# Kernel tuning notes

Measured on AMD Instinct MI355X. Metric: run time of the kernel, lower is better.

The kernel has to match this reference:

```python
import jax, jax.numpy as jnp
import numpy as np

B, S, D = 128, 512, 512  # source requires S == hidden_dim for bmm(Q^T, K^T) to type-check


def setup_inputs() -> dict:
    key = jax.random.key(0)
    ks = jax.random.split(key, 7)
    scale = 1.0 / np.sqrt(D)
    return {
        "x": jax.random.normal(ks[0], (B, S, D), dtype=jnp.float32),
        "Wq": jax.random.uniform(ks[1], (D, D), jnp.float32, -scale, scale),
        "bq": jax.random.uniform(ks[2], (D,), jnp.float32, -scale, scale),
        "Wk": jax.random.uniform(ks[3], (D, D), jnp.float32, -scale, scale),
        "bk": jax.random.uniform(ks[4], (D,), jnp.float32, -scale, scale),
        "Wv": jax.random.uniform(ks[5], (D, D), jnp.float32, -scale, scale),
        "bv": jax.random.uniform(ks[6], (D,), jnp.float32, -scale, scale),
    }


def reference(x, Wq, bq, Wk, bk, Wv, bv):
    # nn.Linear: y = x @ W^T + b
    Q = jnp.einsum("bsd,ed->bse", x, Wq) + bq  # (B,S,D)
    K = jnp.einsum("bsd,ed->bse", x, Wk) + bk
    V = jnp.einsum("bsd,ed->bse", x, Wv) + bv
    Qp = jnp.transpose(Q, (0, 2, 1))  # (B,D,S)
    Kp = jnp.transpose(K, (0, 2, 1))  # (B,D,S); bmm needs S == D
    energy = jnp.matmul(Qp, Kp)       # (B,D,D) -- unscaled, as in source
    attention = jax.nn.softmax(energy, axis=2)
    Vp = jnp.transpose(V, (0, 2, 1))  # (B,D,S)
    context = jnp.matmul(attention, Vp)  # (B,D,S)
    return jnp.transpose(context, (0, 2, 1))  # (B,S,D)
```

## Files before the change

### kernel.cpp

```cpp
#include <hip/hip_runtime.h>
#include <hip/hip_bf16.h>


#define NDIM 512
#define NBATCH 128
constexpr size_t SD = (size_t)NDIM * NDIM;

typedef __attribute__((ext_vector_type(8))) short bf16x8;
typedef __attribute__((ext_vector_type(4))) float f32x4;

typedef const __attribute__((address_space(1))) unsigned int* gas_ptr;
typedef __attribute__((address_space(3))) unsigned int* las_ptr;

struct alignas(8) us4 { unsigned short x, y, z, w; };
struct alignas(4) us2 { unsigned short x, y; };

__device__ __forceinline__ void gl_lds16(const void* g, void* lds) {
    __builtin_amdgcn_global_load_lds((gas_ptr)g, (las_ptr)lds, 16, 0, 0);
}
__device__ __forceinline__ unsigned short f2bf(float x) {
    return __builtin_bit_cast(unsigned short, __float2bfloat16(x));
}
__device__ __forceinline__ float bf2f(unsigned short u) {
    return __bfloat162float(__builtin_bit_cast(__hip_bfloat16, u));
}

template<int EPI, int BIAS>
__global__ __launch_bounds__(512, 2) void gemm8_fused3(
    const unsigned short* aH, const unsigned short* aL, long sA,
    const unsigned short* bH, const unsigned short* bL, long sB,
    void* c0v, void* c1v, long sC, const float* __restrict__ bias)
{
    constexpr int NTK = 16;
    __shared__ unsigned short AHs[2][8192];
    __shared__ unsigned short ALs[2][8192];
    __shared__ unsigned short BHs[2][8192];
    __shared__ unsigned short BLs[2][8192];

    const int nwg = gridDim.x;
    int id = blockIdx.x;
    int wg = ((nwg & 7) == 0) ? ((id & 7) * (nwg >> 3) + (id >> 3)) : id;
    const int z  = wg >> 2;
    const int m0 = ((wg >> 1) & 1) * 256;
    const int n0 = (wg & 1) * 256;

    const int tid = threadIdx.x;
    const int l = tid & 63, w = tid >> 6;
    const int wr = w >> 2, wc = w & 3;

    const unsigned short* gAH = aH + (size_t)z * sA + (size_t)m0 * NDIM;
    const unsigned short* gAL = aL + (size_t)z * sA + (size_t)m0 * NDIM;
    const unsigned short* gBH = bH + (size_t)z * sB + (size_t)n0 * NDIM;
    const unsigned short* gBL = bL + (size_t)z * sB + (size_t)n0 * NDIM;

    auto stage = [&](const unsigned short* g, unsigned short* panel, int kt) {
        const int k0 = kt << 5;
        #pragma unroll
        for (int s = 0; s < 2; ++s) {
            const int G = s * 512 + tid;
            const int r = G >> 2, gp = G & 3;
            gl_lds16(g + (size_t)r * NDIM + k0 + ((gp ^ ((r >> 1) & 3)) << 3),
                     panel + G * 8);
        }
    };
    auto readA = [&](const unsigned short* panel, bf16x8 (&dst)[2][4]) {
        #pragma unroll
        for (int H = 0; H < 2; ++H)
            #pragma unroll
            for (int mi = 0; mi < 4; ++mi) {
                const int row = H * 128 + wr * 64 + mi * 16 + (l & 15);
                const int gp = (l >> 4) ^ ((row >> 1) & 3);
                dst[H][mi] = *(const bf16x8*)&panel[row * 32 + gp * 8];
            }
    };
    auto readB = [&](const unsigned short* panel, bf16x8 (&dst)[2][2]) {
        #pragma unroll
        for (int H = 0; H < 2; ++H)
            #pragma unroll
            for (int ni = 0; ni < 2; ++ni) {
                const int row = H * 128 + wc * 32 + ni * 16 + (l & 15);
                const int gp = (l >> 4) ^ ((row >> 1) & 3);
                dst[H][ni] = *(const bf16x8*)&panel[row * 32 + gp * 8];
            }
    };

    f32x4 acc[2][2][4][2] = {};

    auto mfma32 = [&](const bf16x8 (&a)[2][4], const bf16x8 (&b)[2][2]) {
        __builtin_amdgcn_s_setprio(1);
        #pragma unroll
        for (int Qr = 0; Qr < 2; ++Qr)
            #pragma unroll
            for (int Qc = 0; Qc < 2; ++Qc)
                #pragma unroll
                for (int mi = 0; mi < 4; ++mi)
                    #pragma unroll
                    for (int ni = 0; ni < 2; ++ni)
                        acc[Qr][Qc][mi][ni] = __builtin_amdgcn_mfma_f32_16x16x32_bf16(
                            a[Qr][mi], b[Qc][ni], acc[Qr][Qc][mi][ni], 0, 0, 0);
        __builtin_amdgcn_s_setprio(0);
    };

    stage(gAH, AHs[0], 0); stage(gBH, BHs[0], 0);
    stage(gAL, ALs[0], 0); stage(gBL, BLs[0], 0);
    asm volatile("s_waitcnt vmcnt(4)" ::: "memory");
    asm volatile("s_barrier" ::: "memory");

    for (int kt = 0; kt < NTK; ++kt) {
        const int cur = kt & 1, nxt = cur ^ 1;
        const int ktn = (kt + 1 < NTK) ? kt + 1 : kt;
        bf16x8 ah[2][4], al[2][4], bh[2][2], bl[2][2];

        readA(AHs[cur], ah); readB(BHs[cur], bh);
        stage(gAH, AHs[nxt], ktn); stage(gBH, BHs[nxt], ktn);
        asm volatile("s_waitcnt vmcnt(6)" ::: "memory");
        asm volatile("s_barrier" ::: "memory");
        asm volatile("s_waitcnt lgkmcnt(0)" ::: "memory");
        __builtin_amdgcn_sched_barrier(0);
        mfma32(ah, bh);

        readA(ALs[cur], al);
        stage(gAL, ALs[nxt], ktn);
        asm volatile("s_waitcnt vmcnt(6)" ::: "memory");
        asm volatile("s_barrier" ::: "memory");
        asm volatile("s_waitcnt lgkmcnt(0)" ::: "memory");
        __builtin_amdgcn_sched_barrier(0);
        mfma32(al, bh);

        readB(BLs[cur], bl);
        stage(gBL, BLs[nxt], ktn);
        asm volatile("s_waitcnt vmcnt(4)" ::: "memory");
        asm volatile("s_barrier" ::: "memory");
        asm volatile("s_waitcnt lgkmcnt(0)" ::: "memory");
        __builtin_amdgcn_sched_barrier(0);
        mfma32(ah, bl);
    }
    asm volatile("s_waitcnt vmcnt(0) lgkmcnt(0)" ::: "memory");

    const size_t zc = (size_t)z * sC;
    const int cr = (l >> 4) << 2;
    const int cc = l & 15;
    #pragma unroll
    for (int Qr = 0; Qr < 2; ++Qr) {
        #pragma unroll
        for (int Qc = 0; Qc < 2; ++Qc) {
            #pragma unroll
            for (int mi = 0; mi < 4; ++mi) {
                #pragma unroll
                for (int r = 0; r < 4; ++r) {
                    const int m = m0 + Qr * 128 + wr * 64 + mi * 16 + cr + r;
                    const float bm = (BIAS == 1) ? bias[m] : 0.0f;
                    #pragma unroll
                    for (int ni = 0; ni < 2; ++ni) {
                        const int n = n0 + Qc * 128 + wc * 32 + ni * 16 + cc;
                        float v = acc[Qr][Qc][mi][ni][r] + bm + ((BIAS == 2) ? bias[n] : 0.0f);
                        const size_t idx = zc + (size_t)m * NDIM + n;
                        if (EPI == 0) {
                            ((float*)c0v)[idx] = v;
                        } else if (EPI == 1) {
                            ((unsigned short*)c0v)[idx] = f2bf(v);
                        } else {
                            const unsigned short h = f2bf(v);
                            ((unsigned short*)c0v)[idx] = h;
                            ((unsigned short*)c1v)[idx] = f2bf(v - bf2f(h));
                        }
                    }
                }
            }
        }
    }
}

template<int NSEG, int EPI, int BIAS>
__global__ __launch_bounds__(512, 2) void gemm8_nt(
    const unsigned short* a0, const unsigned short* a1, const unsigned short* a2, long sA,
    const unsigned short* b0, const unsigned short* b1, const unsigned short* b2, long sB,
    void* c0v, void* c1v, long sC, const float* __restrict__ bias)
{
    constexpr int NTK = NSEG * 8;
    __shared__ unsigned short AS[2][256 * 64];
    __shared__ unsigned short BS[2][256 * 64];

    const int nwg = gridDim.x;
    int id = blockIdx.x;
    int wg = ((nwg & 7) == 0) ? ((id & 7) * (nwg >> 3) + (id >> 3)) : id;
    const int z  = wg >> 2;
    const int m0 = ((wg >> 1) & 1) * 256;
    const int n0 = (wg & 1) * 256;

    const int tid = threadIdx.x;
    const int l = tid & 63, w = tid >> 6;
    const int wr = w >> 2, wc = w & 3;

    const size_t zA = (size_t)z * sA + (size_t)m0 * NDIM;
    const size_t zB = (size_t)z * sB + (size_t)n0 * NDIM;

    const int srow = tid >> 3;
    const int scol = (((tid & 7) ^ ((tid >> 3) & 7)) << 3);
    const int ldst = tid * 8;

    auto segA = [&](int s) {
        const unsigned short* p = a0;
        if constexpr (NSEG > 1) { if (s == 1) p = a1; }
        if constexpr (NSEG > 2) { if (s == 2) p = a2; }
        return p;
    };
    auto segB = [&](int s) {
        const unsigned short* p = b0;
        if constexpr (NSEG > 1) { if (s == 1) p = b1; }
        if constexpr (NSEG > 2) { if (s == 2) p = b2; }
        return p;
    };
    auto stageA = [&](int kt, int H, int slot) {
        const int seg = kt >> 3, k0 = (kt & 7) << 6;
        const unsigned short* g = segA(seg) + zA;
        #pragma unroll
        for (int j = 0; j < 2; ++j)
            gl_lds16(g + (size_t)(H * 128 + j * 64 + srow) * NDIM + k0 + scol,
                     &AS[slot][H * 8192 + j * 4096 + ldst]);
    };
    auto stageB = [&](int kt, int H, int slot) {
        const int seg = kt >> 3, k0 = (kt & 7) << 6;
        const unsigned short* g = segB(seg) + zB;
        #pragma unroll
        for (int j = 0; j < 2; ++j)
            gl_lds16(g + (size_t)(H * 128 + j * 64 + srow) * NDIM + k0 + scol,
                     &BS[slot][H * 8192 + j * 4096 + ldst]);
    };

    auto readA = [&](int slot, int H, bf16x8 (&dst)[4][2]) {
        #pragma unroll
        for (int mi = 0; mi < 4; ++mi) {
            const int row = H * 128 + wr * 64 + mi * 16 + (l & 15);
            #pragma unroll
            for (int kk = 0; kk < 2; ++kk) {
                const int s16 = ((kk << 2) + (l >> 4)) ^ (l & 7);
                dst[mi][kk] = *(const bf16x8*)&AS[slot][row * 64 + s16 * 8];
            }
        }
    };
    auto readB = [&](int slot, int H, bf16x8 (&dst)[2][2]) {
        #pragma unroll
        for (int ni = 0; ni < 2; ++ni) {
            const int row = H * 128 + wc * 32 + ni * 16 + (l & 15);
            #pragma unroll
            for (int kk = 0; kk < 2; ++kk) {
                const int s16 = ((kk << 2) + (l >> 4)) ^ (l & 7);
                dst[ni][kk] = *(const bf16x8*)&BS[slot][row * 64 + s16 * 8];
            }
        }
    };
    auto mfma16 = [&](f32x4 (&ac)[4][2], const bf16x8 (&a)[4][2],
                      const bf16x8 (&b)[2][2]) {
        __builtin_amdgcn_s_setprio(1);
        #pragma unroll
        for (int mi = 0; mi < 4; ++mi)
            #pragma unroll
            for (int ni = 0; ni < 2; ++ni)
                #pragma unroll
                for (int kk = 0; kk < 2; ++kk)
                    ac[mi][ni] = __builtin_amdgcn_mfma_f32_16x16x32_bf16(
                        a[mi][kk], b[ni][kk], ac[mi][ni], 0, 0, 0);
        __builtin_amdgcn_s_setprio(0);
    };

    f32x4 acc[2][2][4][2] = {};

    stageA(0, 0, 0); stageB(0, 0, 0); stageB(0, 1, 0); stageA(0, 1, 0);
    asm volatile("s_waitcnt vmcnt(4)" ::: "memory");
    asm volatile("s_barrier" ::: "memory");

    for (int kt = 0; kt < NTK; ++kt) {
        const int cur = kt & 1, nxt = cur ^ 1;
        const int ktn = (kt + 1 < NTK) ? kt + 1 : kt;
        bf16x8 a0f[4][2], a1f[4][2], b0f[2][2], b1f[2][2];

        readA(cur, 0, a0f); readB(cur, 0, b0f);
        stageA(ktn, 0, nxt); stageB(ktn, 0, nxt);
        asm volatile("s_waitcnt vmcnt(6)" ::: "memory");
        asm volatile("s_barrier" ::: "memory");
        asm volatile("s_waitcnt lgkmcnt(0)" ::: "memory");
        __builtin_amdgcn_sched_barrier(0);
        mfma16(acc[0][0], a0f, b0f);

        readB(cur, 1, b1f);
        stageB(ktn, 1, nxt);
        asm volatile("s_waitcnt vmcnt(6)" ::: "memory");
        asm volatile("s_barrier" ::: "memory");
        asm volatile("s_waitcnt lgkmcnt(0)" ::: "memory");
        __builtin_amdgcn_sched_barrier(0);
        mfma16(acc[0][1], a0f, b1f);

        readA(cur, 1, a1f);
        stageA(ktn, 1, nxt);
        asm volatile("s_waitcnt vmcnt(4)" ::: "memory");
        asm volatile("s_barrier" ::: "memory");
        asm volatile("s_waitcnt lgkmcnt(0)" ::: "memory");
        __builtin_amdgcn_sched_barrier(0);
        mfma16(acc[1][1], a1f, b1f);
        mfma16(acc[1][0], a1f, b0f);
    }
    asm volatile("s_waitcnt vmcnt(0) lgkmcnt(0)" ::: "memory");

    const size_t zc = (size_t)z * sC;
    const int cr = (l >> 4) << 2;
    const int cc = l & 15;
    #pragma unroll
    for (int Qr = 0; Qr < 2; ++Qr) {
        #pragma unroll
        for (int Qc = 0; Qc < 2; ++Qc) {
            #pragma unroll
            for (int mi = 0; mi < 4; ++mi) {
                #pragma unroll
                for (int r = 0; r < 4; ++r) {
                    const int m = m0 + Qr * 128 + wr * 64 + mi * 16 + cr + r;
                    const float bm = (BIAS == 1) ? bias[m] : 0.0f;
                    #pragma unroll
                    for (int ni = 0; ni < 2; ++ni) {
                        const int n = n0 + Qc * 128 + wc * 32 + ni * 16 + cc;
                        float v = acc[Qr][Qc][mi][ni][r] + bm + ((BIAS == 2) ? bias[n] : 0.0f);
                        const size_t idx = zc + (size_t)m * NDIM + n;
                        if (EPI == 0) {
                            ((float*)c0v)[idx] = v;
                        } else if (EPI == 1) {
                            ((unsigned short*)c0v)[idx] = f2bf(v);
                        } else {
                            const unsigned short h = f2bf(v);
                            ((unsigned short*)c0v)[idx] = h;
                            ((unsigned short*)c1v)[idx] = f2bf(v - bf2f(h));
                        }
                    }
                }
            }
        }
    }
}

template<int NSEG, int EPI, int BIAS>
__global__ __launch_bounds__(256) void gemm_bf16_nt(
    const unsigned short* a0, const unsigned short* a1, const unsigned short* a2, long sA,
    const unsigned short* b0, const unsigned short* b1, const unsigned short* b2, long sB,
    void* c0v, void* c1v, long sC, const float* __restrict__ bias)
{
    __shared__ unsigned short As[128 * 64];
    __shared__ unsigned short Bs[128 * 64];

    const int z  = blockIdx.z;
    const int m0 = blockIdx.y * 128, n0 = blockIdx.x * 128;
    const int tid = threadIdx.x;
    const int l = tid & 63, w = tid >> 6;
    const int wr = w >> 1, wc = w & 1;

    const int srow = tid >> 3;
    const int scol = (tid & 7) << 3;
    unsigned short* ldsA = &As[tid * 8];
    unsigned short* ldsB = &Bs[tid * 8];

    f32x4 acc[4][4] = {};

    const unsigned short* Asegs[3] = {a0, a1, a2};
    const unsigned short* Bsegs[3] = {b0, b1, b2};

    #pragma unroll
    for (int s = 0; s < NSEG; ++s) {
        const unsigned short* Ab = Asegs[s] + (size_t)z * sA + (size_t)m0 * NDIM;
        const unsigned short* Bb = Bsegs[s] + (size_t)z * sB + (size_t)n0 * NDIM;
        for (int k0 = 0; k0 < NDIM; k0 += 64) {
            __syncthreads();
            #pragma unroll
            for (int i = 0; i < 4; ++i) {
                gl_lds16(Ab + (size_t)(srow + i * 32) * NDIM + k0 + scol, ldsA + i * 2048);
                gl_lds16(Bb + (size_t)(srow + i * 32) * NDIM + k0 + scol, ldsB + i * 2048);
            }
            __syncthreads();
            #pragma unroll
            for (int kk = 0; kk < 2; ++kk) {
                bf16x8 af[4], bfv[4];
                #pragma unroll
                for (int f = 0; f < 4; ++f) {
                    af[f]  = *(const bf16x8*)&As[(wr * 64 + f * 16 + (l & 15)) * 64 + kk * 32 + (l >> 4) * 8];
                    bfv[f] = *(const bf16x8*)&Bs[(wc * 64 + f * 16 + (l & 15)) * 64 + kk * 32 + (l >> 4) * 8];
                }
                #pragma unroll
                for (int mi = 0; mi < 4; ++mi)
                    #pragma unroll
                    for (int ni = 0; ni < 4; ++ni)
                        acc[mi][ni] = __builtin_amdgcn_mfma_f32_16x16x32_bf16(
                            af[mi], bfv[ni], acc[mi][ni], 0, 0, 0);
            }
        }
    }

    const size_t zc = (size_t)z * sC;
    const int cr = (l >> 4) << 2;
    const int cc = l & 15;
    #pragma unroll
    for (int mi = 0; mi < 4; ++mi) {
        #pragma unroll
        for (int r = 0; r < 4; ++r) {
            const int m = m0 + wr * 64 + mi * 16 + cr + r;
            const float bm = (BIAS == 1) ? bias[m] : 0.0f;
            #pragma unroll
            for (int ni = 0; ni < 4; ++ni) {
                const int n = n0 + wc * 64 + ni * 16 + cc;
                float v = acc[mi][ni][r] + bm + ((BIAS == 2) ? bias[n] : 0.0f);
                const size_t idx = zc + (size_t)m * NDIM + n;
                if (EPI == 0) {
                    ((float*)c0v)[idx] = v;
                } else if (EPI == 1) {
                    ((unsigned short*)c0v)[idx] = f2bf(v);
                } else {
                    const unsigned short h = f2bf(v);
                    ((unsigned short*)c0v)[idx] = h;
                    ((unsigned short*)c1v)[idx] = f2bf(v - bf2f(h));
                }
            }
        }
    }
}

__global__ __launch_bounds__(256) void softmax_bf16(
    const float* __restrict__ E, unsigned short* __restrict__ A)
{
    const int l  = threadIdx.x & 63;
    const int wv = threadIdx.x >> 6;
    const size_t row = (size_t)blockIdx.x * 4 + wv;
    const float* p = E + row * NDIM;
    unsigned short* q = A + row * NDIM;

    const float4 v0 = ((const float4*)p)[l * 2];
    const float4 v1 = ((const float4*)p)[l * 2 + 1];

    float mx = fmaxf(fmaxf(fmaxf(v0.x, v0.y), fmaxf(v0.z, v0.w)),
                     fmaxf(fmaxf(v1.x, v1.y), fmaxf(v1.z, v1.w)));
    #pragma unroll
    for (int s = 32; s > 0; s >>= 1) mx = fmaxf(mx, __shfl_xor(mx, s, 64));

    float e0 = __expf(v0.x - mx), e1 = __expf(v0.y - mx);
    float e2 = __expf(v0.z - mx), e3 = __expf(v0.w - mx);
    float e4 = __expf(v1.x - mx), e5 = __expf(v1.y - mx);
    float e6 = __expf(v1.z - mx), e7 = __expf(v1.w - mx);
    float sm = ((e0 + e1) + (e2 + e3)) + ((e4 + e5) + (e6 + e7));
    #pragma unroll
    for (int s = 32; s > 0; s >>= 1) sm += __shfl_xor(sm, s, 64);

    const float inv = 1.0f / sm;
    us4 o0, o1;
    o0.x = f2bf(e0 * inv); o0.y = f2bf(e1 * inv);
    o0.z = f2bf(e2 * inv); o0.w = f2bf(e3 * inv);
    o1.x = f2bf(e4 * inv); o1.y = f2bf(e5 * inv);
    o1.z = f2bf(e6 * inv); o1.w = f2bf(e7 * inv);
    ((us4*)q)[l * 2]     = o0;
    ((us4*)q)[l * 2 + 1] = o1;
}

template<bool LO>
__global__ __launch_bounds__(256) void split_to_bf16(
    const float* __restrict__ src,
    unsigned short* __restrict__ hi, unsigned short* __restrict__ lo, int n4)
{
    const int i = blockIdx.x * 256 + threadIdx.x;
    if (i >= n4) return;
    const float4 v = ((const float4*)src)[i];
    us4 h;
    h.x = f2bf(v.x); h.y = f2bf(v.y); h.z = f2bf(v.z); h.w = f2bf(v.w);
    ((us4*)hi)[i] = h;
    if (LO) {
        us4 g;
        g.x = f2bf(v.x - bf2f(h.x)); g.y = f2bf(v.y - bf2f(h.y));
        g.z = f2bf(v.z - bf2f(h.z)); g.w = f2bf(v.w - bf2f(h.w));
        ((us4*)lo)[i] = g;
    }
}

extern "C" void kernel_launch(void* const* d_in, const int* in_sizes, int n_in,
                              void* d_out, int out_size, void* d_ws, size_t ws_size,
                              hipStream_t stream)
{
    const float* x  = (const float*)d_in[0];
    const float* Wq = (const float*)d_in[1];
    const float* bq = (const float*)d_in[2];
    const float* Wk = (const float*)d_in[3];
    const float* bk = (const float*)d_in[4];
    const float* Wv = (const float*)d_in[5];
    const float* bv = (const float*)d_in[6];
    float* out = (float*)d_out;

    long units = (long)(ws_size / (2 * SD));
    long cl = (units - 6) / 10;
    if (cl < 1) cl = 1;
    int c = 1;
    while (c * 2 <= cl && c < 128) c *= 2;
    const bool use8 = (c >= 64);
    if (!use8 && c > 32) c = 32;

    unsigned short* p = (unsigned short*)d_ws;
    auto take = [&](size_t elems) { unsigned short* r = p; p += elems; return r; };
    unsigned short* WqH = take(SD);
    unsigned short* WqL = take(SD);
    unsigned short* WkH = take(SD);
    unsigned short* WkL = take(SD);
    unsigned short* WvH = take(SD);
    unsigned short* xH  = take((size_t)c * SD);
    unsigned short* xL  = take((size_t)c * SD);
    unsigned short* QH  = take((size_t)c * SD);
    unsigned short* QL  = take((size_t)c * SD);
    unsigned short* KH  = take((size_t)c * SD);
    unsigned short* KL  = take((size_t)c * SD);
    unsigned short* Vb  = take((size_t)c * SD);
    unsigned short* Ab  = take((size_t)c * SD);
    float* Ew = (float*)p;

    const int n4w = (int)(SD / 4);
    split_to_bf16<true ><<<dim3((n4w + 255) / 256), dim3(256), 0, stream>>>(Wq, WqH, WqL, n4w);
    split_to_bf16<true ><<<dim3((n4w + 255) / 256), dim3(256), 0, stream>>>(Wk, WkH, WkL, n4w);
    split_to_bf16<false><<<dim3((n4w + 255) / 256), dim3(256), 0, stream>>>(Wv, WvH, nullptr, n4w);

    for (int b0 = 0; b0 < NBATCH; b0 += c) {
        const int cb = (NBATCH - b0 < c) ? (NBATCH - b0) : c;
        const int n4 = (int)((size_t)cb * SD / 4);
        split_to_bf16<true><<<dim3((n4 + 255) / 256), dim3(256), 0, stream>>>(
            x + (size_t)b0 * SD, xH, xL, n4);

        if (use8) {
            const dim3 g(4 * cb), blk(512);
            gemm8_fused3<2, 1><<<g, blk, 0, stream>>>(
                WqH, WqL, 0,  xH, xL, (long)SD,  QH, QL, (long)SD, bq);
            gemm8_fused3<2, 2><<<g, blk, 0, stream>>>(
                xH, xL, (long)SD,  WkH, WkL, 0,  KH, KL, (long)SD, bk);
            gemm8_nt<1, 1, 2><<<g, blk, 0, stream>>>(
                xH, nullptr, nullptr, (long)SD,  WvH, nullptr, nullptr, 0,  Vb, nullptr, (long)SD, bv);
            gemm8_fused3<0, 0><<<g, blk, 0, stream>>>(
                QH, QL, (long)SD,  KH, KL, (long)SD,  Ew, nullptr, (long)SD, nullptr);
            softmax_bf16<<<dim3(cb * NDIM / 4), dim3(256), 0, stream>>>(Ew, Ab);
            gemm8_nt<1, 0, 0><<<g, blk, 0, stream>>>(
                Vb, nullptr, nullptr, (long)SD,  Ab, nullptr, nullptr, (long)SD,
                out + (size_t)b0 * SD, nullptr, (long)SD, nullptr);
        } else {
            const dim3 g(4, 4, cb), blk(256);
            gemm_bf16_nt<3, 2, 1><<<g, blk, 0, stream>>>(
                WqH, WqL, WqH, 0,  xH, xH, xL, (long)SD,  QH, QL, (long)SD, bq);
            gemm_bf16_nt<3, 2, 2><<<g, blk, 0, stream>>>(
                xH, xL, xH, (long)SD,  WkH, WkH, WkL, 0,  KH, KL, (long)SD, bk);
            gemm_bf16_nt<1, 1, 2><<<g, blk, 0, stream>>>(
                xH, nullptr, nullptr, (long)SD,  WvH, nullptr, nullptr, 0,  Vb, nullptr, (long)SD, bv);
            gemm_bf16_nt<3, 0, 0><<<g, blk, 0, stream>>>(
                QH, QL, QH, (long)SD,  KH, KH, KL, (long)SD,  Ew, nullptr, (long)SD, nullptr);
            softmax_bf16<<<dim3(cb * NDIM / 4), dim3(256), 0, stream>>>(Ew, Ab);
            gemm_bf16_nt<1, 0, 0><<<g, blk, 0, stream>>>(
                Vb, nullptr, nullptr, (long)SD,  Ab, nullptr, nullptr, (long)SD,
                out + (size_t)b0 * SD, nullptr, (long)SD, nullptr);
        }
    }
}
```

Measured before the change: 520.8 us.

## Fuse partial softmax into energy GEMM epilogue with per-half row stats

```diff
diff --git a/kernel.cpp b/kernel.cpp
--- a/kernel.cpp
+++ b/kernel.cpp
@@ -13,7 +13,6 @@
 typedef __attribute__((address_space(3))) unsigned int* las_ptr;
 
 struct alignas(8) us4 { unsigned short x, y, z, w; };
-struct alignas(4) us2 { unsigned short x, y; };
 
 __device__ __forceinline__ void gl_lds16(const void* g, void* lds) {
     __builtin_amdgcn_global_load_lds((gas_ptr)g, (las_ptr)lds, 16, 0, 0);
@@ -140,6 +139,77 @@
     const size_t zc = (size_t)z * sC;
     const int cr = (l >> 4) << 2;
     const int cc = l & 15;
+
+    if constexpr (EPI == 3) {
+        float* red  = (float*)&AHs[0][0];
+        float* red2 = red + 1024;
+        float2* stats = (float2*)c1v;
+        const int h = n0 >> 8;
+        __syncthreads();
+        #pragma unroll
+        for (int Qr = 0; Qr < 2; ++Qr)
+            #pragma unroll
+            for (int mi = 0; mi < 4; ++mi)
+                #pragma unroll
+                for (int r = 0; r < 4; ++r) {
+                    float v = fmaxf(fmaxf(acc[Qr][0][mi][0][r], acc[Qr][0][mi][1][r]),
+                                    fmaxf(acc[Qr][1][mi][0][r], acc[Qr][1][mi][1][r]));
+                    #pragma unroll
+                    for (int s = 1; s < 16; s <<= 1) v = fmaxf(v, __shfl_xor(v, s, 64));
+                    const int row = Qr * 128 + wr * 64 + mi * 16 + cr + r;
+                    if ((l & 15) == 0) red[row * 4 + wc] = v;
+                }
+        __syncthreads();
+        #pragma unroll
+        for (int Qr = 0; Qr < 2; ++Qr)
+            #pragma unroll
+            for (int mi = 0; mi < 4; ++mi)
+                #pragma unroll
+                for (int r = 0; r < 4; ++r) {
+                    const int row = Qr * 128 + wr * 64 + mi * 16 + cr + r;
+                    const float mb = fmaxf(fmaxf(red[row * 4], red[row * 4 + 1]),
+                                           fmaxf(red[row * 4 + 2], red[row * 4 + 3]));
+                    float sum = 0.0f;
+                    #pragma unroll
+                    for (int Qc = 0; Qc < 2; ++Qc)
+                        #pragma unroll
+                        for (int ni = 0; ni < 2; ++ni) {
+                            const float e = __expf(acc[Qr][Qc][mi][ni][r] - mb);
+                            acc[Qr][Qc][mi][ni][r] = e;
+                            sum += e;
+                        }
+                    #pragma unroll
+                    for (int s = 1; s < 16; s <<= 1) sum += __shfl_xor(sum, s, 64);
+                    if ((l & 15) == 0) red2[row * 4 + wc] = sum;
+                }
+        __syncthreads();
+        #pragma unroll
+        for (int Qr = 0; Qr < 2; ++Qr)
+            #pragma unroll
+            for (int mi = 0; mi < 4; ++mi)
+                #pragma unroll
+                for (int r = 0; r < 4; ++r) {
+                    const int row = Qr * 128 + wr * 64 + mi * 16 + cr + r;
+                    if (wc == 0 && (l & 15) == 0) {
+                        const float mb = fmaxf(fmaxf(red[row * 4], red[row * 4 + 1]),
+                                               fmaxf(red[row * 4 + 2], red[row * 4 + 3]));
+                        const float sb = red2[row * 4] + red2[row * 4 + 1]
+                                       + red2[row * 4 + 2] + red2[row * 4 + 3];
+                        stats[((size_t)z * NDIM + m0 + row) * 2 + h] = make_float2(mb, sb);
+                    }
+                    const int m = m0 + row;
+                    #pragma unroll
+                    for (int Qc = 0; Qc < 2; ++Qc)
+                        #pragma unroll
+                        for (int ni = 0; ni < 2; ++ni) {
+                            const int n = n0 + Qc * 128 + wc * 32 + ni * 16 + cc;
+                            ((unsigned short*)c0v)[zc + (size_t)m * NDIM + n] =
+                                f2bf(acc[Qr][Qc][mi][ni][r]);
+                        }
+                }
+        return;
+    }
+
     #pragma unroll
     for (int Qr = 0; Qr < 2; ++Qr) {
         #pragma unroll
@@ -160,9 +230,9 @@
                         } else if (EPI == 1) {
                             ((unsigned short*)c0v)[idx] = f2bf(v);
                         } else {
-                            const unsigned short h = f2bf(v);
-                            ((unsigned short*)c0v)[idx] = h;
-                            ((unsigned short*)c1v)[idx] = f2bf(v - bf2f(h));
+                            const unsigned short hh = f2bf(v);
+                            ((unsigned short*)c0v)[idx] = hh;
+                            ((unsigned short*)c1v)[idx] = f2bf(v - bf2f(hh));
                         }
                     }
                 }
@@ -325,9 +395,9 @@
                         } else if (EPI == 1) {
                             ((unsigned short*)c0v)[idx] = f2bf(v);
                         } else {
-                            const unsigned short h = f2bf(v);
-                            ((unsigned short*)c0v)[idx] = h;
-                            ((unsigned short*)c1v)[idx] = f2bf(v - bf2f(h));
+                            const unsigned short hh = f2bf(v);
+                            ((unsigned short*)c0v)[idx] = hh;
+                            ((unsigned short*)c1v)[idx] = f2bf(v - bf2f(hh));
                         }
                     }
                 }
@@ -410,13 +480,36 @@
                 } else if (EPI == 1) {
                     ((unsigned short*)c0v)[idx] = f2bf(v);
                 } else {
-                    const unsigned short h = f2bf(v);
-                    ((unsigned short*)c0v)[idx] = h;
-                    ((unsigned short*)c1v)[idx] = f2bf(v - bf2f(h));
+                    const unsigned short hh = f2bf(v);
+                    ((unsigned short*)c0v)[idx] = hh;
+                    ((unsigned short*)c1v)[idx] = f2bf(v - bf2f(hh));
                 }
             }
         }
     }
+}
+
+__global__ __launch_bounds__(256) void scaleP(
+    unsigned short* __restrict__ P, const float2* __restrict__ stats)
+{
+    const int l  = threadIdx.x & 63;
+    const int wv = threadIdx.x >> 6;
+    const size_t row = (size_t)blockIdx.x * 4 + wv;
+    unsigned short* p = P + row * NDIM;
+
+    const float2 st0 = stats[row * 2];
+    const float2 st1 = stats[row * 2 + 1];
+    const float M = fmaxf(st0.x, st1.x);
+    const float S = st0.y * __expf(st0.x - M) + st1.y * __expf(st1.x - M);
+    const float f = __expf(((l < 32) ? st0.x : st1.x) - M) / S;
+
+    us4 a = ((us4*)p)[l * 2], b = ((us4*)p)[l * 2 + 1];
+    a.x = f2bf(bf2f(a.x) * f); a.y = f2bf(bf2f(a.y) * f);
+    a.z = f2bf(bf2f(a.z) * f); a.w = f2bf(bf2f(a.w) * f);
+    b.x = f2bf(bf2f(b.x) * f); b.y = f2bf(bf2f(b.y) * f);
+    b.z = f2bf(bf2f(b.z) * f); b.w = f2bf(bf2f(b.w) * f);
+    ((us4*)p)[l * 2]     = a;
+    ((us4*)p)[l * 2 + 1] = b;
 }
 
 __global__ __launch_bounds__(256) void softmax_bf16(
@@ -487,7 +580,7 @@
     float* out = (float*)d_out;
 
     long units = (long)(ws_size / (2 * SD));
-    long cl = (units - 6) / 10;
+    long cl = (units - 7) / 10;
     if (cl < 1) cl = 1;
     int c = 1;
     while (c * 2 <= cl && c < 128) c *= 2;
@@ -509,6 +602,8 @@
     unsigned short* KL  = take((size_t)c * SD);
     unsigned short* Vb  = take((size_t)c * SD);
     unsigned short* Ab  = take((size_t)c * SD);
+    unsigned short* stats_u = take((size_t)c * 4096);
+    float2* stats = (float2*)stats_u;
     float* Ew = (float*)p;
 
     const int n4w = (int)(SD / 4);
@@ -530,9 +625,9 @@
                 xH, xL, (long)SD,  WkH, WkL, 0,  KH, KL, (long)SD, bk);
             gemm8_nt<1, 1, 2><<<g, blk, 0, stream>>>(
                 xH, nullptr, nullptr, (long)SD,  WvH, nullptr, nullptr, 0,  Vb, nullptr, (long)SD, bv);
-            gemm8_fused3<0, 0><<<g, blk, 0, stream>>>(
-                QH, QL, (long)SD,  KH, KL, (long)SD,  Ew, nullptr, (long)SD, nullptr);
-            softmax_bf16<<<dim3(cb * NDIM / 4), dim3(256), 0, stream>>>(Ew, Ab);
+            gemm8_fused3<3, 0><<<g, blk, 0, stream>>>(
+                QH, QL, (long)SD,  KH, KL, (long)SD,  Ab, stats, (long)SD, nullptr);
+            scaleP<<<dim3(cb * NDIM / 4), dim3(256), 0, stream>>>(Ab, stats);
             gemm8_nt<1, 0, 0><<<g, blk, 0, stream>>>(
                 Vb, nullptr, nullptr, (long)SD,  Ab, nullptr, nullptr, (long)SD,
                 out + (size_t)b0 * SD, nullptr, (long)SD, nullptr);
```

After: 529.6 us. About the same (+1.7%).
